# Kernel optimization log

Measured on AMD Instinct MI355X. Metric: run time of the kernel, lower is better.

## Reference

```python
import jax, jax.numpy as jnp
import numpy as np

REG_WEIGHT = 1.0
VAR_WEIGHT = 0.01
B, J, H, W = 128, 16, 128, 128

# Flattened skeleton edge list (4 groups of sizes 4,4,2,2 -> 12 edges)
ID1 = np.array([0, 1, 3, 4, 10, 11, 13, 14, 2, 3, 12, 13])
ID2 = np.array([1, 2, 4, 5, 11, 12, 14, 15, 6, 6, 8, 8])
GID = np.array([0, 0, 0, 0, 1, 1, 1, 1, 2, 2, 3, 3])
WSK = np.array([1.0085885098415446, 1.0, 1.0, 1.0085885098415446,
                1.1375361376887123, 1.0, 1.0, 1.1375361376887123,
                1.0, 1.0, 1.0, 1.0], dtype=np.float32)
NGROUPS = 4


def setup_inputs() -> dict:
    key = jax.random.key(0)
    k1, k2, k3, k4 = jax.random.split(key, 4)
    output = jax.random.normal(k1, (B, J, H, W), dtype=jnp.float32)
    mask = jnp.zeros((B, J), dtype=jnp.int32)
    ind = jax.random.randint(k2, (B, J), 0, J * H * W, dtype=jnp.int32)
    target = jax.random.normal(k3, (B, J, 1), dtype=jnp.float32)
    gt_2d = jax.random.normal(k4, (B, 2 * J), dtype=jnp.float32)
    return {"output": output, "mask": mask, "ind": ind, "target": target, "gt_2d": gt_2d}


def _gather_pred(output, ind):
    # permute(0,2,3,1) then flatten -> [B, H*W*C], gather along dim 1
    b = output.shape[0]
    feat = jnp.transpose(output, (0, 2, 3, 1)).reshape(b, -1)
    return jnp.take_along_axis(feat, ind, axis=1)[..., None]  # [B, J, 1]


def _reg_loss(pred, target, mask):
    num = mask.astype(jnp.float32).sum()
    m = mask.astype(jnp.float32)[..., None]  # [B,J,1]
    d = pred * m - target * m
    ad = jnp.abs(d)
    sl1 = jnp.where(ad < 1.0, 0.5 * d * d, ad - 0.5).sum()  # smooth_l1, sum
    return sl1 / (num + 0.0001)


def _var_loss(pred, visible, mask, gt_2d):
    xy = jax.lax.stop_gradient(gt_2d.reshape(gt_2d.shape[0], -1, 2))  # original backward gives no grad to gt_2d
    inp = pred[..., 0]          # [B,J]
    vis = visible[..., 0]       # [B,J]
    id1, id2, gid = jnp.asarray(ID1), jnp.asarray(ID2), jnp.asarray(GID)
    w = jnp.asarray(WSK)
    v = (vis[:, id1] > 0.5) & (vis[:, id2] > 0.5)  # [B,12] visibility of both endpoints
    d2d = ((xy[:, id1] - xy[:, id2]) ** 2).sum(-1)  # [B,12]
    dz = (inp[:, id1] - inp[:, id2]) ** 2
    s = jnp.where(v, d2d + dz, 1.0)                 # safe sqrt arg
    l = jnp.where(v, jnp.sqrt(s) * w, 0.0)          # [B,12] weighted bone lengths
    G = (gid[:, None] == jnp.arange(NGROUPS)[None, :]).astype(jnp.float32)  # [12,4]
    num = v.astype(jnp.float32) @ G                 # [B,4]
    sum_l = l @ G                                   # [B,4]
    E = jnp.where(num >= 0.5, sum_l / jnp.maximum(num, 1.0), 0.0)  # group mean length
    E_e = E[:, gid]
    n_e = jnp.maximum(num[:, gid], 1.0)
    loss_j = jnp.where(v, (l - E_e) ** 2 / (2.0 * n_e), 0.0)  # [B,12]
    active = (mask.sum(axis=1) == 0).astype(jnp.float32)      # [B]
    total = (loss_j.sum(-1) * active).sum()
    return VAR_WEIGHT * total / pred.shape[0]


def reference(output, mask, ind, target, gt_2d):
    pred = _gather_pred(output, ind)
    loss = jnp.zeros((), dtype=jnp.float32)
    if REG_WEIGHT > 0:
        loss = loss + REG_WEIGHT * _reg_loss(pred, target, mask)
    if VAR_WEIGHT > 0:
        loss = loss + _var_loss(pred, target, mask, gt_2d)
    return loss
```

## Files before the change

### kernel.cpp

```cpp
#include <hip/hip_runtime.h>


#define NB 128
#define NJ 16
#define NH 128
#define NW 128
#define NE 12
#define NG 4

__global__ __launch_bounds__(128) void fusion_loss_kernel(
    const float* __restrict__ output,
    const int*   __restrict__ mask,
    const int*   __restrict__ ind,
    const float* __restrict__ target,
    const float* __restrict__ gt2d,
    float*       __restrict__ out)
{
    const int b = threadIdx.x;

    const int   id1[NE] = {0,1,3,4,10,11,13,14,2,3,12,13};
    const int   id2[NE] = {1,2,4,5,11,12,14,15,6,6,8,8};
    const int   gid[NE] = {0,0,0,0,1,1,1,1,2,2,3,3};
    const float wsk[NE] = {1.0085885098415446f, 1.0f, 1.0f, 1.0085885098415446f,
                           1.1375361376887123f, 1.0f, 1.0f, 1.1375361376887123f,
                           1.0f, 1.0f, 1.0f, 1.0f};

    const int*   indb = ind    + b * NJ;
    const float* tb   = target + b * NJ;
    const int*   mb   = mask   + b * NJ;
    const float* gb   = gt2d   + b * 2 * NJ;
    const float* ob   = output + (size_t)b * NJ * NH * NW;

    float pred[NJ], vis[NJ];
    int   msk[NJ];
    float xy0[NJ], xy1[NJ];
#pragma unroll
    for (int j = 0; j < NJ; ++j) {
        int t  = indb[j];
        int jj = t & (NJ - 1);
        int hw = t >> 4;
        pred[j] = ob[jj * (NH * NW) + hw];
        vis[j]  = tb[j];
        msk[j]  = mb[j];
        xy0[j]  = gb[2 * j];
        xy1[j]  = gb[2 * j + 1];
    }

    float sl1  = 0.0f;
    float numm = 0.0f;
    int   masksum = 0;
#pragma unroll
    for (int j = 0; j < NJ; ++j) {
        float m  = (float)msk[j];
        float d  = pred[j] * m - vis[j] * m;
        float ad = fabsf(d);
        sl1  += (ad < 1.0f) ? 0.5f * d * d : ad - 0.5f;
        numm += m;
        masksum += msk[j];
    }

    float gnum[NG] = {0.f, 0.f, 0.f, 0.f};
    float gsum[NG] = {0.f, 0.f, 0.f, 0.f};
    float lv[NE];
    bool  vv[NE];
#pragma unroll
    for (int e = 0; e < NE; ++e) {
        const int a = id1[e], c = id2[e];
        const bool v = (vis[a] > 0.5f) && (vis[c] > 0.5f);
        float dx  = xy0[a] - xy0[c];
        float dy  = xy1[a] - xy1[c];
        float d2d = dx * dx + dy * dy;
        float dzv = pred[a] - pred[c];
        float s   = v ? (d2d + dzv * dzv) : 1.0f;
        float l   = v ? sqrtf(s) * wsk[e] : 0.0f;
        lv[e] = l;
        vv[e] = v;
        gnum[gid[e]] += v ? 1.0f : 0.0f;
        gsum[gid[e]] += l;
    }

    float E[NG];
#pragma unroll
    for (int g = 0; g < NG; ++g)
        E[g] = (gnum[g] >= 0.5f) ? gsum[g] / fmaxf(gnum[g], 1.0f) : 0.0f;

    float tot = 0.0f;
#pragma unroll
    for (int e = 0; e < NE; ++e) {
        if (vv[e]) {
            float ne = fmaxf(gnum[gid[e]], 1.0f);
            float dd = lv[e] - E[gid[e]];
            tot += dd * dd / (2.0f * ne);
        }
    }
    if (masksum != 0) tot = 0.0f;

#pragma unroll
    for (int off = 32; off > 0; off >>= 1) {
        sl1  += __shfl_down(sl1,  off, 64);
        numm += __shfl_down(numm, off, 64);
        tot  += __shfl_down(tot,  off, 64);
    }
    __shared__ float s_sl1[2], s_num[2], s_tot[2];
    const int wave = threadIdx.x >> 6;
    const int lane = threadIdx.x & 63;
    if (lane == 0) { s_sl1[wave] = sl1; s_num[wave] = numm; s_tot[wave] = tot; }
    __syncthreads();
    if (threadIdx.x == 0) {
        float S = s_sl1[0] + s_sl1[1];
        float N = s_num[0] + s_num[1];
        float T = s_tot[0] + s_tot[1];
        out[0] = S / (N + 0.0001f) + 0.01f * T / 128.0f;
    }
}

extern "C" void kernel_launch(void* const* d_in, const int* in_sizes, int n_in,
                              void* d_out, int out_size, void* d_ws, size_t ws_size,
                              hipStream_t stream) {
    const float* output = (const float*)d_in[0];
    const int*   mask   = (const int*)  d_in[1];
    const int*   ind    = (const int*)  d_in[2];
    const float* target = (const float*)d_in[3];
    const float* gt2d   = (const float*)d_in[4];
    float*       out    = (float*)d_out;

    fusion_loss_kernel<<<1, 128, 0, stream>>>(output, mask, ind, target, gt2d, out);
}
```

Measured before the change: 170.6 us.

## Spread per-sample gathers across eight threads per batch row with LDS exchange

The kernel now launches 1024 threads instead of 128, so eight threads share each batch sample and each issues two of the sixteen scattered gathers into the large output tensor. Gathered predictions go into padded shared memory, and after a barrier one thread per sample computes the bone-length variance term using vectorized loads of target, mask and gt_2d. The aim is to issue many more independent random memory loads at once and hide the latency of the serialized per-thread gather chain. In exchange it adds a block barrier, 16-wave reduction overhead and idle lanes during the variance phase.

```diff
diff --git a/kernel.cpp b/kernel.cpp
--- a/kernel.cpp
+++ b/kernel.cpp
@@ -1,14 +1,12 @@
 #include <hip/hip_runtime.h>
 
 
-#define NB 128
 #define NJ 16
-#define NH 128
-#define NW 128
 #define NE 12
 #define NG 4
+#define LDSS 17
 
-__global__ __launch_bounds__(128) void fusion_loss_kernel(
+__global__ __launch_bounds__(1024) void fusion_loss_kernel(
     const float* __restrict__ output,
     const int*   __restrict__ mask,
     const int*   __restrict__ ind,
@@ -16,84 +14,103 @@
     const float* __restrict__ gt2d,
     float*       __restrict__ out)
 {
-    const int b = threadIdx.x;
+    const int tid = threadIdx.x;
+    const int b   = tid >> 3;
+    const int sub = tid & 7;
 
-    const int   id1[NE] = {0,1,3,4,10,11,13,14,2,3,12,13};
-    const int   id2[NE] = {1,2,4,5,11,12,14,15,6,6,8,8};
-    const int   gid[NE] = {0,0,0,0,1,1,1,1,2,2,3,3};
-    const float wsk[NE] = {1.0085885098415446f, 1.0f, 1.0f, 1.0085885098415446f,
-                           1.1375361376887123f, 1.0f, 1.0f, 1.1375361376887123f,
-                           1.0f, 1.0f, 1.0f, 1.0f};
+    __shared__ float s_pred[128 * LDSS];
+    __shared__ float s_red[16][3];
 
-    const int*   indb = ind    + b * NJ;
-    const float* tb   = target + b * NJ;
-    const int*   mb   = mask   + b * NJ;
-    const float* gb   = gt2d   + b * 2 * NJ;
-    const float* ob   = output + (size_t)b * NJ * NH * NW;
+    const int j0 = sub, j1 = sub + 8;
 
-    float pred[NJ], vis[NJ];
-    int   msk[NJ];
-    float xy0[NJ], xy1[NJ];
+    const int t0 = ind[b * NJ + j0];
+    const int t1 = ind[b * NJ + j1];
+    const float v0 = target[b * NJ + j0];
+    const float v1 = target[b * NJ + j1];
+    const int   m0 = mask[b * NJ + j0];
+    const int   m1 = mask[b * NJ + j1];
+
+    float tg[NJ]; int mk[NJ]; float g2[2 * NJ];
+    if (sub == 0) {
+        const float4* tp = (const float4*)(target + b * NJ);
+        const int4*   mp = (const int4*)  (mask   + b * NJ);
+        const float4* gp = (const float4*)(gt2d   + b * 2 * NJ);
 #pragma unroll
-    for (int j = 0; j < NJ; ++j) {
-        int t  = indb[j];
-        int jj = t & (NJ - 1);
-        int hw = t >> 4;
-        pred[j] = ob[jj * (NH * NW) + hw];
-        vis[j]  = tb[j];
-        msk[j]  = mb[j];
-        xy0[j]  = gb[2 * j];
-        xy1[j]  = gb[2 * j + 1];
+        for (int k = 0; k < 4; ++k) {
+            float4 tv = tp[k];
+            tg[4*k] = tv.x; tg[4*k+1] = tv.y; tg[4*k+2] = tv.z; tg[4*k+3] = tv.w;
+            int4 mv = mp[k];
+            mk[4*k] = mv.x; mk[4*k+1] = mv.y; mk[4*k+2] = mv.z; mk[4*k+3] = mv.w;
+        }
+#pragma unroll
+        for (int k = 0; k < 8; ++k) {
+            float4 gv = gp[k];
+            g2[4*k] = gv.x; g2[4*k+1] = gv.y; g2[4*k+2] = gv.z; g2[4*k+3] = gv.w;
+        }
     }
 
-    float sl1  = 0.0f;
-    float numm = 0.0f;
-    int   masksum = 0;
-#pragma unroll
-    for (int j = 0; j < NJ; ++j) {
-        float m  = (float)msk[j];
-        float d  = pred[j] * m - vis[j] * m;
-        float ad = fabsf(d);
-        sl1  += (ad < 1.0f) ? 0.5f * d * d : ad - 0.5f;
-        numm += m;
-        masksum += msk[j];
+    const float* ob = output + (size_t)b * (NJ * 128 * 128);
+    const float p0 = ob[(t0 & (NJ - 1)) * (128 * 128) + (t0 >> 4)];
+    const float p1 = ob[(t1 & (NJ - 1)) * (128 * 128) + (t1 >> 4)];
+    s_pred[b * LDSS + j0] = p0;
+    s_pred[b * LDSS + j1] = p1;
+
+    float sl1 = 0.0f, numm = 0.0f;
+    {
+        float m = (float)m0, d = p0 * m - v0 * m, ad = fabsf(d);
+        sl1 += (ad < 1.0f) ? 0.5f * d * d : ad - 0.5f;  numm += m;
+        m = (float)m1; d = p1 * m - v1 * m; ad = fabsf(d);
+        sl1 += (ad < 1.0f) ? 0.5f * d * d : ad - 0.5f;  numm += m;
     }
 
-    float gnum[NG] = {0.f, 0.f, 0.f, 0.f};
-    float gsum[NG] = {0.f, 0.f, 0.f, 0.f};
-    float lv[NE];
-    bool  vv[NE];
-#pragma unroll
-    for (int e = 0; e < NE; ++e) {
-        const int a = id1[e], c = id2[e];
-        const bool v = (vis[a] > 0.5f) && (vis[c] > 0.5f);
-        float dx  = xy0[a] - xy0[c];
-        float dy  = xy1[a] - xy1[c];
-        float d2d = dx * dx + dy * dy;
-        float dzv = pred[a] - pred[c];
-        float s   = v ? (d2d + dzv * dzv) : 1.0f;
-        float l   = v ? sqrtf(s) * wsk[e] : 0.0f;
-        lv[e] = l;
-        vv[e] = v;
-        gnum[gid[e]] += v ? 1.0f : 0.0f;
-        gsum[gid[e]] += l;
-    }
-
-    float E[NG];
-#pragma unroll
-    for (int g = 0; g < NG; ++g)
-        E[g] = (gnum[g] >= 0.5f) ? gsum[g] / fmaxf(gnum[g], 1.0f) : 0.0f;
+    __syncthreads();
 
     float tot = 0.0f;
+    if (sub == 0) {
+        const int   id1[NE] = {0,1,3,4,10,11,13,14,2,3,12,13};
+        const int   id2[NE] = {1,2,4,5,11,12,14,15,6,6,8,8};
+        const int   gid[NE] = {0,0,0,0,1,1,1,1,2,2,3,3};
+        const float wsk[NE] = {1.0085885098415446f, 1.0f, 1.0f, 1.0085885098415446f,
+                               1.1375361376887123f, 1.0f, 1.0f, 1.1375361376887123f,
+                               1.0f, 1.0f, 1.0f, 1.0f};
+        float pr[NJ];
 #pragma unroll
-    for (int e = 0; e < NE; ++e) {
-        if (vv[e]) {
-            float ne = fmaxf(gnum[gid[e]], 1.0f);
-            float dd = lv[e] - E[gid[e]];
-            tot += dd * dd / (2.0f * ne);
+        for (int j = 0; j < NJ; ++j) pr[j] = s_pred[b * LDSS + j];
+
+        float gnum[NG] = {0.f,0.f,0.f,0.f};
+        float gsum[NG] = {0.f,0.f,0.f,0.f};
+        float lv[NE]; bool vvv[NE];
+#pragma unroll
+        for (int e = 0; e < NE; ++e) {
+            const int a = id1[e], c = id2[e];
+            const bool v = (tg[a] > 0.5f) && (tg[c] > 0.5f);
+            float dx = g2[2*a] - g2[2*c];
+            float dy = g2[2*a+1] - g2[2*c+1];
+            float d2d = dx * dx + dy * dy;
+            float dz  = pr[a] - pr[c];
+            float s   = v ? (d2d + dz * dz) : 1.0f;
+            float l   = v ? sqrtf(s) * wsk[e] : 0.0f;
+            lv[e] = l; vvv[e] = v;
+            gnum[gid[e]] += v ? 1.0f : 0.0f;
+            gsum[gid[e]] += l;
         }
+        float E[NG];
+#pragma unroll
+        for (int g = 0; g < NG; ++g)
+            E[g] = (gnum[g] >= 0.5f) ? gsum[g] / fmaxf(gnum[g], 1.0f) : 0.0f;
+#pragma unroll
+        for (int e = 0; e < NE; ++e) {
+            if (vvv[e]) {
+                float ne = fmaxf(gnum[gid[e]], 1.0f);
+                float dd = lv[e] - E[gid[e]];
+                tot += dd * dd / (2.0f * ne);
+            }
+        }
+        int msum = 0;
+#pragma unroll
+        for (int j = 0; j < NJ; ++j) msum += mk[j];
+        if (msum != 0) tot = 0.0f;
     }
-    if (masksum != 0) tot = 0.0f;
 
 #pragma unroll
     for (int off = 32; off > 0; off >>= 1) {
@@ -101,15 +118,13 @@
         numm += __shfl_down(numm, off, 64);
         tot  += __shfl_down(tot,  off, 64);
     }
-    __shared__ float s_sl1[2], s_num[2], s_tot[2];
-    const int wave = threadIdx.x >> 6;
-    const int lane = threadIdx.x & 63;
-    if (lane == 0) { s_sl1[wave] = sl1; s_num[wave] = numm; s_tot[wave] = tot; }
+    const int wave = tid >> 6, lane = tid & 63;
+    if (lane == 0) { s_red[wave][0] = sl1; s_red[wave][1] = numm; s_red[wave][2] = tot; }
     __syncthreads();
-    if (threadIdx.x == 0) {
-        float S = s_sl1[0] + s_sl1[1];
-        float N = s_num[0] + s_num[1];
-        float T = s_tot[0] + s_tot[1];
+    if (tid == 0) {
+        float S = 0.f, N = 0.f, T = 0.f;
+#pragma unroll
+        for (int w = 0; w < 16; ++w) { S += s_red[w][0]; N += s_red[w][1]; T += s_red[w][2]; }
         out[0] = S / (N + 0.0001f) + 0.01f * T / 128.0f;
     }
 }
@@ -124,5 +139,5 @@
     const float* gt2d   = (const float*)d_in[4];
     float*       out    = (float*)d_out;
 
-    fusion_loss_kernel<<<1, 128, 0, stream>>>(output, mask, ind, target, gt2d, out);
+    fusion_loss_kernel<<<1, 1024, 0, stream>>>(output, mask, ind, target, gt2d, out);
 }
```

After: 172.5 us. About the same (+1.1%).
